# Kernel optimization log

Hardware: AMD Instinct MI355X
Metric: run time of the kernel (lower is better)

The kernel has to match this reference:

```python
import jax, jax.numpy as jnp
import numpy as np


def setup_inputs() -> dict:
    key = jax.random.key(0)
    kq, kk, kv, km = jax.random.split(key, 4)
    b, h, w, c = 4, 128, 512, 128
    num_splits = 8
    win = w // num_splits  # 64
    q = jax.random.normal(kq, (b, h * w, c), dtype=jnp.float32)
    k = jax.random.normal(kk, (b, h * w, c), dtype=jnp.float32)
    v = jax.random.normal(kv, (b, h * w, c), dtype=jnp.float32)
    attn_mask = jax.random.normal(km, (num_splits, win, win), dtype=jnp.float32)
    return {"q": q, "k": k, "v": v, "attn_mask": attn_mask,
            "h": h, "w": w, "num_splits": num_splits}


def reference(q, k, v, attn_mask, h, w, num_splits):
    # with_shift=True branch (attn_mask is only consumed when shifting)
    b, hw, c = q.shape
    assert hw == h * w
    win = w // num_splits
    shift = win // 2
    scale = c ** 0.5

    def prep(x):
        # [b, h*w, c] -> rows of width w, shifted, then split into windows
        x = x.reshape(b * h, w, c)
        x = jnp.roll(x, -shift, axis=1)
        return x.reshape(b * h, num_splits, win, c)

    qs, ks, vs = prep(q), prep(k), prep(v)
    scores = jnp.einsum('bsqc,bskc->bsqk', qs, ks) / scale
    scores = scores + attn_mask[None]  # broadcast over b*h (== torch repeat)
    attn = jax.nn.softmax(scores, axis=-1)
    out = jnp.einsum('bsqk,bskc->bsqc', attn, vs)
    # merge windows back to rows: [b, h, w, c]
    out = out.reshape(b, h, w, c)
    out = jnp.roll(out, shift, axis=2)  # undo shift along w
    return out.reshape(b, h * w, c)
```

## Files before the change

kernel.cpp:

```cpp
#include <hip/hip_runtime.h>

#define BH      512
#define W_ROWS  512
#define C_DIM   128
#define NSPLIT  8
#define WIN     64
#define SHIFT   32

typedef __attribute__((ext_vector_type(8))) short  short8;
typedef __attribute__((ext_vector_type(4))) float  floatx4;

__device__ __forceinline__ ushort f2bf(float x) {
    union { float f; unsigned u; } c; c.f = x;
    unsigned u = c.u;
    return (ushort)((u + 0x7FFFu + ((u >> 16) & 1u)) >> 16);
}

__global__ __launch_bounds__(256, 4)
void swin_attn_kernel(const float* __restrict__ qg,
                      const float* __restrict__ kg,
                      const float* __restrict__ vg,
                      const float* __restrict__ mg,
                      float* __restrict__ og)
{
    __shared__ __align__(16) ushort sK[64][136];
    __shared__ __align__(16) char   sVt[128 * 144];

    const int tid  = threadIdx.x;
    const int bh   = blockIdx.x >> 3;
    const int s    = blockIdx.x & 7;
    const int wv   = tid >> 6;
    const int lane = tid & 63;
    const int l16  = lane & 15;
    const int quad = lane >> 4;

    const size_t base = (size_t)bh * (W_ROWS * C_DIM);

    const int j  = tid & 31;
    const int h  = tid >> 5;
    const int c0 = j * 4;
    const int r0 = h * 8;

    floatx4 kr[8], vr[8];
    #pragma unroll
    for (int i = 0; i < 8; ++i) {
        const int rg = (s * WIN + r0 + i + SHIFT) & (W_ROWS - 1);
        kr[i] = *(const floatx4*)(kg + base + (size_t)rg * C_DIM + c0);
    }
    #pragma unroll
    for (int i = 0; i < 8; ++i) {
        const int rg = (s * WIN + r0 + i + SHIFT) & (W_ROWS - 1);
        vr[i] = *(const floatx4*)(vg + base + (size_t)rg * C_DIM + c0);
    }
    const int qrow = wv * 16 + l16;
    const int rgq  = (s * WIN + qrow + SHIFT) & (W_ROWS - 1);
    const float* qp = qg + base + (size_t)rgq * C_DIM + quad * 8;
    floatx4 qa[4], qb[4];
    #pragma unroll
    for (int kk = 0; kk < 4; ++kk) {
        qa[kk] = *(const floatx4*)(qp + kk * 32);
        qb[kk] = *(const floatx4*)(qp + kk * 32 + 4);
    }

    #pragma unroll
    for (int i = 0; i < 8; ++i) {
        ushort4 kb;
        kb.x = f2bf(kr[i][0]); kb.y = f2bf(kr[i][1]);
        kb.z = f2bf(kr[i][2]); kb.w = f2bf(kr[i][3]);
        *(ushort4*)&sK[r0 + i][c0] = kb;
    }
    #pragma unroll
    for (int m = 0; m < 4; ++m) {
        short8 col;
        #pragma unroll
        for (int i = 0; i < 8; ++i) col[i] = (short)f2bf(vr[i][m]);
        const int chnk = h ^ (j & 7);
        *(short8*)(sVt + (size_t)(c0 + m) * 144 + chnk * 16) = col;
    }
    short8 qf[4];
    #pragma unroll
    for (int kk = 0; kk < 4; ++kk) {
        short8 f;
        f[0] = (short)f2bf(qa[kk][0]); f[1] = (short)f2bf(qa[kk][1]);
        f[2] = (short)f2bf(qa[kk][2]); f[3] = (short)f2bf(qa[kk][3]);
        f[4] = (short)f2bf(qb[kk][0]); f[5] = (short)f2bf(qb[kk][1]);
        f[6] = (short)f2bf(qb[kk][2]); f[7] = (short)f2bf(qb[kk][3]);
        qf[kk] = f;
    }
    __syncthreads();

    floatx4 acc[4];
    const floatx4 fz = {0.f, 0.f, 0.f, 0.f};
    #pragma unroll
    for (int t = 0; t < 4; ++t) acc[t] = fz;

    #pragma unroll
    for (int kk = 0; kk < 4; ++kk) {
        const int ch0 = kk * 32 + quad * 8;
        #pragma unroll
        for (int t = 0; t < 4; ++t) {
            short8 bf = *(const short8*)&sK[t * 16 + l16][ch0];
            acc[t] = __builtin_amdgcn_mfma_f32_16x16x32_bf16(qf[kk], bf, acc[t], 0, 0, 0);
        }
    }

    const float* mrow = mg + s * (WIN * WIN);
    float pr[4][4];
    #pragma unroll
    for (int r = 0; r < 4; ++r) {
        const int qw = wv * 16 + quad * 4 + r;
        float mx = -3.0e38f;
        #pragma unroll
        for (int t = 0; t < 4; ++t) {
            float val = acc[t][r] * 0.08838834764831845f
                      + mrow[qw * WIN + t * 16 + l16];
            pr[t][r] = val;
            mx = fmaxf(mx, val);
        }
        mx = fmaxf(mx, __shfl_xor(mx, 1));
        mx = fmaxf(mx, __shfl_xor(mx, 2));
        mx = fmaxf(mx, __shfl_xor(mx, 4));
        mx = fmaxf(mx, __shfl_xor(mx, 8));
        float sum = 0.f;
        #pragma unroll
        for (int t = 0; t < 4; ++t) {
            float e = __expf(pr[t][r] - mx);
            pr[t][r] = e;
            sum += e;
        }
        sum += __shfl_xor(sum, 1);
        sum += __shfl_xor(sum, 2);
        sum += __shfl_xor(sum, 4);
        sum += __shfl_xor(sum, 8);
        float rs = 1.0f / sum;
        #pragma unroll
        for (int t = 0; t < 4; ++t) pr[t][r] *= rs;
    }

    __syncthreads();
    ushort* sP = (ushort*)&sK[0][0];
    #pragma unroll
    for (int r = 0; r < 4; ++r) {
        const int qw = wv * 16 + quad * 4 + r;
        #pragma unroll
        for (int t = 0; t < 4; ++t)
            sP[qw * 72 + t * 16 + l16] = f2bf(pr[t][r]);
    }
    __syncthreads();

    floatx4 o[8];
    #pragma unroll
    for (int t = 0; t < 8; ++t) o[t] = fz;
    #pragma unroll
    for (int kk = 0; kk < 2; ++kk) {
        short8 pf = *(const short8*)&sP[(wv * 16 + l16) * 72 + kk * 32 + quad * 8];
        #pragma unroll
        for (int t = 0; t < 8; ++t) {
            const int ch   = t * 16 + l16;
            const int chnk = (kk * 4 + quad) ^ ((ch >> 2) & 7);
            short8 vf = *(const short8*)(sVt + (size_t)ch * 144 + chnk * 16);
            o[t] = __builtin_amdgcn_mfma_f32_16x16x32_bf16(pf, vf, o[t], 0, 0, 0);
        }
    }

    #pragma unroll
    for (int r = 0; r < 4; ++r) {
        const int qw = wv * 16 + quad * 4 + r;
        const int rg = (s * WIN + qw + SHIFT) & (W_ROWS - 1);
        float* op = og + base + (size_t)rg * C_DIM + l16;
        #pragma unroll
        for (int t = 0; t < 8; ++t)
            op[t * 16] = o[t][r];
    }
}

extern "C" void kernel_launch(void* const* d_in, const int* in_sizes, int n_in,
                              void* d_out, int out_size, void* d_ws, size_t ws_size,
                              hipStream_t stream) {
    const float* q = (const float*)d_in[0];
    const float* k = (const float*)d_in[1];
    const float* v = (const float*)d_in[2];
    const float* m = (const float*)d_in[3];
    float* out = (float*)d_out;
    dim3 grid(BH * NSPLIT), block(256);
    hipLaunchKernelGGL(swin_attn_kernel, grid, block, 0, stream, q, k, v, m, out);
}
```

Baseline: 395.7 us.

## Make blocks persistent over 8 rows with register-prefetched next-window loads

```diff
diff --git a/kernel.cpp b/kernel.cpp
--- a/kernel.cpp
+++ b/kernel.cpp
@@ -6,6 +6,7 @@
 #define NSPLIT  8
 #define WIN     64
 #define SHIFT   32
+#define NW      8
 
 typedef __attribute__((ext_vector_type(8))) short  short8;
 typedef __attribute__((ext_vector_type(4))) float  floatx4;
@@ -16,7 +17,7 @@
     return (ushort)((u + 0x7FFFu + ((u >> 16) & 1u)) >> 16);
 }
 
-__global__ __launch_bounds__(256, 4)
+__global__ __launch_bounds__(256, 2)
 void swin_attn_kernel(const float* __restrict__ qg,
                       const float* __restrict__ kg,
                       const float* __restrict__ vg,
@@ -25,152 +26,188 @@
 {
     __shared__ __align__(16) ushort sK[64][136];
     __shared__ __align__(16) char   sVt[128 * 144];
+    __shared__ __align__(16) ushort sP[64][72];
 
     const int tid  = threadIdx.x;
-    const int bh   = blockIdx.x >> 3;
     const int s    = blockIdx.x & 7;
+    const int bh0  = (blockIdx.x >> 3) * NW;
     const int wv   = tid >> 6;
     const int lane = tid & 63;
     const int l16  = lane & 15;
     const int quad = lane >> 4;
 
-    const size_t base = (size_t)bh * (W_ROWS * C_DIM);
-
     const int j  = tid & 31;
     const int h  = tid >> 5;
     const int c0 = j * 4;
     const int r0 = h * 8;
 
-    floatx4 kr[8], vr[8];
+    int kvoff[8];
     #pragma unroll
-    for (int i = 0; i < 8; ++i) {
-        const int rg = (s * WIN + r0 + i + SHIFT) & (W_ROWS - 1);
-        kr[i] = *(const floatx4*)(kg + base + (size_t)rg * C_DIM + c0);
-    }
-    #pragma unroll
-    for (int i = 0; i < 8; ++i) {
-        const int rg = (s * WIN + r0 + i + SHIFT) & (W_ROWS - 1);
-        vr[i] = *(const floatx4*)(vg + base + (size_t)rg * C_DIM + c0);
-    }
+    for (int i = 0; i < 8; ++i)
+        kvoff[i] = ((s * WIN + r0 + i + SHIFT) & (W_ROWS - 1)) * C_DIM + c0;
+
     const int qrow = wv * 16 + l16;
-    const int rgq  = (s * WIN + qrow + SHIFT) & (W_ROWS - 1);
-    const float* qp = qg + base + (size_t)rgq * C_DIM + quad * 8;
-    floatx4 qa[4], qb[4];
-    #pragma unroll
-    for (int kk = 0; kk < 4; ++kk) {
-        qa[kk] = *(const floatx4*)(qp + kk * 32);
-        qb[kk] = *(const floatx4*)(qp + kk * 32 + 4);
-    }
-
-    #pragma unroll
-    for (int i = 0; i < 8; ++i) {
-        ushort4 kb;
-        kb.x = f2bf(kr[i][0]); kb.y = f2bf(kr[i][1]);
-        kb.z = f2bf(kr[i][2]); kb.w = f2bf(kr[i][3]);
-        *(ushort4*)&sK[r0 + i][c0] = kb;
-    }
-    #pragma unroll
-    for (int m = 0; m < 4; ++m) {
-        short8 col;
-        #pragma unroll
-        for (int i = 0; i < 8; ++i) col[i] = (short)f2bf(vr[i][m]);
-        const int chnk = h ^ (j & 7);
-        *(short8*)(sVt + (size_t)(c0 + m) * 144 + chnk * 16) = col;
-    }
-    short8 qf[4];
-    #pragma unroll
-    for (int kk = 0; kk < 4; ++kk) {
-        short8 f;
-        f[0] = (short)f2bf(qa[kk][0]); f[1] = (short)f2bf(qa[kk][1]);
-        f[2] = (short)f2bf(qa[kk][2]); f[3] = (short)f2bf(qa[kk][3]);
-        f[4] = (short)f2bf(qb[kk][0]); f[5] = (short)f2bf(qb[kk][1]);
-        f[6] = (short)f2bf(qb[kk][2]); f[7] = (short)f2bf(qb[kk][3]);
-        qf[kk] = f;
-    }
-    __syncthreads();
-
-    floatx4 acc[4];
-    const floatx4 fz = {0.f, 0.f, 0.f, 0.f};
-    #pragma unroll
-    for (int t = 0; t < 4; ++t) acc[t] = fz;
-
-    #pragma unroll
-    for (int kk = 0; kk < 4; ++kk) {
-        const int ch0 = kk * 32 + quad * 8;
-        #pragma unroll
-        for (int t = 0; t < 4; ++t) {
-            short8 bf = *(const short8*)&sK[t * 16 + l16][ch0];
-            acc[t] = __builtin_amdgcn_mfma_f32_16x16x32_bf16(qf[kk], bf, acc[t], 0, 0, 0);
-        }
-    }
-
-    const float* mrow = mg + s * (WIN * WIN);
-    float pr[4][4];
+    const int qoff = ((s * WIN + qrow + SHIFT) & (W_ROWS - 1)) * C_DIM + quad * 8;
+
+    int ooff[4];
     #pragma unroll
     for (int r = 0; r < 4; ++r) {
         const int qw = wv * 16 + quad * 4 + r;
-        float mx = -3.0e38f;
-        #pragma unroll
-        for (int t = 0; t < 4; ++t) {
-            float val = acc[t][r] * 0.08838834764831845f
-                      + mrow[qw * WIN + t * 16 + l16];
-            pr[t][r] = val;
-            mx = fmaxf(mx, val);
-        }
-        mx = fmaxf(mx, __shfl_xor(mx, 1));
-        mx = fmaxf(mx, __shfl_xor(mx, 2));
-        mx = fmaxf(mx, __shfl_xor(mx, 4));
-        mx = fmaxf(mx, __shfl_xor(mx, 8));
-        float sum = 0.f;
-        #pragma unroll
-        for (int t = 0; t < 4; ++t) {
-            float e = __expf(pr[t][r] - mx);
-            pr[t][r] = e;
-            sum += e;
-        }
-        sum += __shfl_xor(sum, 1);
-        sum += __shfl_xor(sum, 2);
-        sum += __shfl_xor(sum, 4);
-        sum += __shfl_xor(sum, 8);
-        float rs = 1.0f / sum;
-        #pragma unroll
-        for (int t = 0; t < 4; ++t) pr[t][r] *= rs;
-    }
-
+        ooff[r] = ((s * WIN + qw + SHIFT) & (W_ROWS - 1)) * C_DIM + l16;
+    }
+
+    float mk[4][4];
+    {
+        const float* mrow = mg + s * (WIN * WIN);
+        #pragma unroll
+        for (int r = 0; r < 4; ++r) {
+            const int qw = wv * 16 + quad * 4 + r;
+            #pragma unroll
+            for (int t = 0; t < 4; ++t)
+                mk[r][t] = mrow[qw * WIN + t * 16 + l16];
+        }
+    }
+
+    floatx4 kr[8], vr[8], qa[4], qb[4];
+    short8  qf[4];
+    const floatx4 fz = {0.f, 0.f, 0.f, 0.f};
+
+    auto stage_write = [&]() {
+        #pragma unroll
+        for (int i = 0; i < 8; ++i) {
+            ushort4 kb;
+            kb.x = f2bf(kr[i][0]); kb.y = f2bf(kr[i][1]);
+            kb.z = f2bf(kr[i][2]); kb.w = f2bf(kr[i][3]);
+            *(ushort4*)&sK[r0 + i][c0] = kb;
+        }
+        #pragma unroll
+        for (int m = 0; m < 4; ++m) {
+            short8 col;
+            #pragma unroll
+            for (int i = 0; i < 8; ++i) col[i] = (short)f2bf(vr[i][m]);
+            const int chnk = h ^ (j & 7);
+            *(short8*)(sVt + (size_t)(c0 + m) * 144 + chnk * 16) = col;
+        }
+        #pragma unroll
+        for (int kk = 0; kk < 4; ++kk) {
+            short8 f;
+            f[0] = (short)f2bf(qa[kk][0]); f[1] = (short)f2bf(qa[kk][1]);
+            f[2] = (short)f2bf(qa[kk][2]); f[3] = (short)f2bf(qa[kk][3]);
+            f[4] = (short)f2bf(qb[kk][0]); f[5] = (short)f2bf(qb[kk][1]);
+            f[6] = (short)f2bf(qb[kk][2]); f[7] = (short)f2bf(qb[kk][3]);
+            qf[kk] = f;
+        }
+    };
+
+    {
+        const size_t base = (size_t)bh0 * (W_ROWS * C_DIM);
+        #pragma unroll
+        for (int i = 0; i < 8; ++i) kr[i] = *(const floatx4*)(kg + base + kvoff[i]);
+        #pragma unroll
+        for (int i = 0; i < 8; ++i) vr[i] = *(const floatx4*)(vg + base + kvoff[i]);
+        #pragma unroll
+        for (int kk = 0; kk < 4; ++kk) {
+            qa[kk] = *(const floatx4*)(qg + base + qoff + kk * 32);
+            qb[kk] = *(const floatx4*)(qg + base + qoff + kk * 32 + 4);
+        }
+    }
+    stage_write();
     __syncthreads();
-    ushort* sP = (ushort*)&sK[0][0];
-    #pragma unroll
-    for (int r = 0; r < 4; ++r) {
-        const int qw = wv * 16 + quad * 4 + r;
-        #pragma unroll
-        for (int t = 0; t < 4; ++t)
-            sP[qw * 72 + t * 16 + l16] = f2bf(pr[t][r]);
-    }
-    __syncthreads();
-
-    floatx4 o[8];
-    #pragma unroll
-    for (int t = 0; t < 8; ++t) o[t] = fz;
-    #pragma unroll
-    for (int kk = 0; kk < 2; ++kk) {
-        short8 pf = *(const short8*)&sP[(wv * 16 + l16) * 72 + kk * 32 + quad * 8];
-        #pragma unroll
-        for (int t = 0; t < 8; ++t) {
-            const int ch   = t * 16 + l16;
-            const int chnk = (kk * 4 + quad) ^ ((ch >> 2) & 7);
-            short8 vf = *(const short8*)(sVt + (size_t)ch * 144 + chnk * 16);
-            o[t] = __builtin_amdgcn_mfma_f32_16x16x32_bf16(pf, vf, o[t], 0, 0, 0);
-        }
-    }
-
-    #pragma unroll
-    for (int r = 0; r < 4; ++r) {
-        const int qw = wv * 16 + quad * 4 + r;
-        const int rg = (s * WIN + qw + SHIFT) & (W_ROWS - 1);
-        float* op = og + base + (size_t)rg * C_DIM + l16;
-        #pragma unroll
-        for (int t = 0; t < 8; ++t)
-            op[t * 16] = o[t][r];
+
+    for (int w = 0; w < NW; ++w) {
+        if (w + 1 < NW) {
+            const size_t basen = (size_t)(bh0 + w + 1) * (W_ROWS * C_DIM);
+            #pragma unroll
+            for (int i = 0; i < 8; ++i) kr[i] = *(const floatx4*)(kg + basen + kvoff[i]);
+            #pragma unroll
+            for (int i = 0; i < 8; ++i) vr[i] = *(const floatx4*)(vg + basen + kvoff[i]);
+            #pragma unroll
+            for (int kk = 0; kk < 4; ++kk) {
+                qa[kk] = *(const floatx4*)(qg + basen + qoff + kk * 32);
+                qb[kk] = *(const floatx4*)(qg + basen + qoff + kk * 32 + 4);
+            }
+        }
+
+        floatx4 acc[4];
+        #pragma unroll
+        for (int t = 0; t < 4; ++t) acc[t] = fz;
+        #pragma unroll
+        for (int kk = 0; kk < 4; ++kk) {
+            const int ch0 = kk * 32 + quad * 8;
+            #pragma unroll
+            for (int t = 0; t < 4; ++t) {
+                short8 bf = *(const short8*)&sK[t * 16 + l16][ch0];
+                acc[t] = __builtin_amdgcn_mfma_f32_16x16x32_bf16(qf[kk], bf, acc[t], 0, 0, 0);
+            }
+        }
+
+        float pr[4][4];
+        #pragma unroll
+        for (int r = 0; r < 4; ++r) {
+            float mx = -3.0e38f;
+            #pragma unroll
+            for (int t = 0; t < 4; ++t) {
+                float val = acc[t][r] * 0.08838834764831845f + mk[r][t];
+                pr[t][r] = val;
+                mx = fmaxf(mx, val);
+            }
+            mx = fmaxf(mx, __shfl_xor(mx, 1));
+            mx = fmaxf(mx, __shfl_xor(mx, 2));
+            mx = fmaxf(mx, __shfl_xor(mx, 4));
+            mx = fmaxf(mx, __shfl_xor(mx, 8));
+            float sum = 0.f;
+            #pragma unroll
+            for (int t = 0; t < 4; ++t) {
+                float e = __expf(pr[t][r] - mx);
+                pr[t][r] = e;
+                sum += e;
+            }
+            sum += __shfl_xor(sum, 1);
+            sum += __shfl_xor(sum, 2);
+            sum += __shfl_xor(sum, 4);
+            sum += __shfl_xor(sum, 8);
+            float rs = 1.0f / sum;
+            #pragma unroll
+            for (int t = 0; t < 4; ++t) pr[t][r] *= rs;
+        }
+
+        #pragma unroll
+        for (int r = 0; r < 4; ++r) {
+            const int qw = wv * 16 + quad * 4 + r;
+            #pragma unroll
+            for (int t = 0; t < 4; ++t)
+                sP[qw][t * 16 + l16] = f2bf(pr[t][r]);
+        }
+
+        floatx4 o[8];
+        #pragma unroll
+        for (int t = 0; t < 8; ++t) o[t] = fz;
+        #pragma unroll
+        for (int kk = 0; kk < 2; ++kk) {
+            short8 pf = *(const short8*)&sP[wv * 16 + l16][kk * 32 + quad * 8];
+            #pragma unroll
+            for (int t = 0; t < 8; ++t) {
+                const int ch   = t * 16 + l16;
+                const int chnk = (kk * 4 + quad) ^ ((ch >> 2) & 7);
+                short8 vf = *(const short8*)(sVt + (size_t)ch * 144 + chnk * 16);
+                o[t] = __builtin_amdgcn_mfma_f32_16x16x32_bf16(pf, vf, o[t], 0, 0, 0);
+            }
+        }
+
+        {
+            const size_t baseo = (size_t)(bh0 + w) * (W_ROWS * C_DIM);
+            #pragma unroll
+            for (int r = 0; r < 4; ++r) {
+                float* op = og + baseo + ooff[r];
+                #pragma unroll
+                for (int t = 0; t < 8; ++t)
+                    op[t * 16] = o[t][r];
+            }
+        }
+
+        __syncthreads();
+        if (w + 1 < NW) stage_write();
+        __syncthreads();
     }
 }
 
@@ -182,6 +219,6 @@
     const float* v = (const float*)d_in[2];
     const float* m = (const float*)d_in[3];
     float* out = (float*)d_out;
-    dim3 grid(BH * NSPLIT), block(256);
+    dim3 grid(BH * NSPLIT / NW), block(256);
     hipLaunchKernelGGL(swin_attn_kernel, grid, block, 0, stream, q, k, v, m, out);
 }
```

After: 398.8 us. No clear change (+0.8%).
